# Optimization experiments

Measured on AMD Instinct MI355X. Metric: run time of the kernel, lower is better.

## Reference

```python
import jax, jax.numpy as jnp
import numpy as np

N = 50000   # num nodes
E = 600000  # num edges per signed adjacency
D = 128     # feature dim
K = 10      # num_diff_layers
C = 0.15    # restart probability


def setup_inputs() -> dict:
    key = jax.random.key(0)
    ks = jax.random.split(key, 8)
    rows_p = jax.random.randint(ks[0], (E,), 0, N, dtype=jnp.int32)
    cols_p = jax.random.randint(ks[1], (E,), 0, N, dtype=jnp.int32)
    vals_p = jax.random.uniform(ks[2], (E,), dtype=jnp.float32)
    rows_m = jax.random.randint(ks[3], (E,), 0, N, dtype=jnp.int32)
    cols_m = jax.random.randint(ks[4], (E,), 0, N, dtype=jnp.int32)
    vals_m = jax.random.uniform(ks[5], (E,), dtype=jnp.float32)
    X = jax.random.normal(ks[6], (N, D), dtype=jnp.float32)
    # torch code draws old_M ~ Uniform(-1, 1) at forward time; we expose it as input
    M0 = jax.random.uniform(ks[7], (N, D), dtype=jnp.float32, minval=-1.0, maxval=1.0)
    return {"rows_p": rows_p, "cols_p": cols_p, "vals_p": vals_p,
            "rows_m": rows_m, "cols_m": cols_m, "vals_m": vals_m,
            "X": X, "M0": M0}


def _spmm(rows, cols, vals, dense):
    # COO sparse [N,N] @ dense [N,D]: gather columns, scale, scatter-add to rows
    return jax.ops.segment_sum(vals[:, None] * dense[cols], rows,
                               num_segments=dense.shape[0])


def reference(rows_p, cols_p, vals_p, rows_m, cols_m, vals_m, X, M0):
    tilda_X = C * X  # restart term
    P, M = X, M0
    for _ in range(K):
        new_P = _spmm(rows_p, cols_p, vals_p, P) + _spmm(rows_m, cols_m, vals_m, M) + tilda_X
        new_M = _spmm(rows_m, cols_m, vals_m, P) + _spmm(rows_p, cols_p, vals_p, M)
        P, M = new_P, new_M
    return (P, M)
```

## Files before the change

kernel.cpp:

```cpp
#include <hip/hip_runtime.h>
#include <math.h>


#define TB 256

__device__ __forceinline__ unsigned pack_bf16(float a, float b) {
    unsigned ua = __float_as_uint(a), ub = __float_as_uint(b);
    ua += 0x7fffu + ((ua >> 16) & 1u);
    ub += 0x7fffu + ((ub >> 16) & 1u);
    return (ua >> 16) | (ub & 0xffff0000u);
}

__device__ __forceinline__ float2 unpack_bf16(unsigned w) {
    float2 r;
    r.x = __uint_as_float(w << 16);
    r.y = __uint_as_float(w & 0xffff0000u);
    return r;
}

__global__ void zero_int_kernel(int* __restrict__ p, int n) {
    int i = blockIdx.x * blockDim.x + threadIdx.x;
    if (i < n) p[i] = 0;
}

__global__ void hist2_kernel(const int* __restrict__ rows_p, const int* __restrict__ rows_m,
                             int E, int* __restrict__ cnt) {
    int e = blockIdx.x * blockDim.x + threadIdx.x;
    if (e < 2 * E) {
        int r = (e < E) ? rows_p[e] : rows_m[e - E];
        atomicAdd(&cnt[r], 1);
    }
}

__global__ void scanA_kernel(const int* __restrict__ cnt, int* __restrict__ bsum, int n) {
    __shared__ int wsum[16];
    int tid = threadIdx.x, lane = tid & 63, wid = tid >> 6;
    int i = blockIdx.x * 1024 + tid;
    int x = (i < n) ? cnt[i] : 0;
#pragma unroll
    for (int o = 1; o < 64; o <<= 1) { int y = __shfl_up(x, o); if (lane >= o) x += y; }
    if (lane == 63) wsum[wid] = x;
    __syncthreads();
    if (tid == 0) {
        int s = 0;
#pragma unroll
        for (int w = 0; w < 16; ++w) s += wsum[w];
        bsum[blockIdx.x] = s;
    }
}

__global__ void scanB_kernel(int* __restrict__ bsum, int nb) {
    __shared__ int wsum[16];
    int tid = threadIdx.x, lane = tid & 63, wid = tid >> 6;
    int x = (tid < nb) ? bsum[tid] : 0;
    int incl = x;
#pragma unroll
    for (int o = 1; o < 64; o <<= 1) { int y = __shfl_up(incl, o); if (lane >= o) incl += y; }
    if (lane == 63) wsum[wid] = incl;
    __syncthreads();
    if (wid == 0) {
        int s = (lane < 16) ? wsum[lane] : 0;
#pragma unroll
        for (int o = 1; o < 16; o <<= 1) { int y = __shfl_up(s, o); if (lane >= o) s += y; }
        if (lane < 16) wsum[lane] = s;
    }
    __syncthreads();
    int base = (wid > 0) ? wsum[wid - 1] : 0;
    if (tid < nb) bsum[tid] = base + incl - x;
}

__global__ void scanC_kernel(const int* __restrict__ cnt, const int* __restrict__ bsum,
                             int* __restrict__ off, int* __restrict__ cur, int n) {
    __shared__ int wsum[16];
    int tid = threadIdx.x, lane = tid & 63, wid = tid >> 6;
    int i = blockIdx.x * 1024 + tid;
    int x = (i < n) ? cnt[i] : 0;
    int incl = x;
#pragma unroll
    for (int o = 1; o < 64; o <<= 1) { int y = __shfl_up(incl, o); if (lane >= o) incl += y; }
    if (lane == 63) wsum[wid] = incl;
    __syncthreads();
    if (wid == 0) {
        int s = (lane < 16) ? wsum[lane] : 0;
#pragma unroll
        for (int o = 1; o < 16; o <<= 1) { int y = __shfl_up(s, o); if (lane >= o) s += y; }
        if (lane < 16) wsum[lane] = s;
    }
    __syncthreads();
    int base = bsum[blockIdx.x] + ((wid > 0) ? wsum[wid - 1] : 0);
    if (i < n) {
        int ex = base + incl - x;
        off[i] = ex;
        cur[i] = ex;
        if (i == n - 1) off[n] = base + incl;
    }
}

__global__ void fill2_kernel(const int* __restrict__ rows_p, const int* __restrict__ cols_p,
                             const float* __restrict__ vals_p,
                             const int* __restrict__ rows_m, const int* __restrict__ cols_m,
                             const float* __restrict__ vals_m, int E,
                             int* __restrict__ cur, int2* __restrict__ edge) {
    int e = blockIdx.x * blockDim.x + threadIdx.x;
    if (e < 2 * E) {
        int r, c; float v;
        if (e < E) { r = rows_p[e]; c = cols_p[e]; v =  vals_p[e]; }
        else       { r = rows_m[e - E]; c = cols_m[e - E]; v = -vals_m[e - E]; }
        int p = atomicAdd(&cur[r], 1);
        edge[p] = make_int2(c, __float_as_int(v));
    }
}

__global__ void init_kernel(const float* __restrict__ X, const float* __restrict__ M0,
                            unsigned* __restrict__ Sb, unsigned* __restrict__ Db,
                            unsigned* __restrict__ tXb, int n) {
    int i = blockIdx.x * blockDim.x + threadIdx.x;
    if (i < n) {
        float2 x = ((const float2*)X)[i];
        float2 m = ((const float2*)M0)[i];
        Sb[i]  = pack_bf16(x.x + m.x, x.y + m.y);
        Db[i]  = pack_bf16(x.x - m.x, x.y - m.y);
        tXb[i] = pack_bf16(0.15f * x.x, 0.15f * x.y);
    }
}

__global__ void final_kernel(const unsigned* __restrict__ Sb, const unsigned* __restrict__ Db,
                             float* __restrict__ P, float* __restrict__ M, int n) {
    int i = blockIdx.x * blockDim.x + threadIdx.x;
    if (i < n) {
        float2 s = unpack_bf16(Sb[i]);
        float2 d = unpack_bf16(Db[i]);
        ((float2*)P)[i] = make_float2(0.5f * (s.x + d.x), 0.5f * (s.y + d.y));
        ((float2*)M)[i] = make_float2(0.5f * (s.x - d.x), 0.5f * (s.y - d.y));
    }
}

__global__ __launch_bounds__(TB) void layer_kernel(
    const int* __restrict__ off, const int2* __restrict__ edge,
    const unsigned* __restrict__ Sin, const unsigned* __restrict__ Din,
    unsigned* __restrict__ Sout, unsigned* __restrict__ Dout,
    const unsigned* __restrict__ tXb, int N) {
    int b = blockIdx.x;
    int slot = b & 7;
    int sys = slot >> 2;
    int r4 = (b >> 3) * 4 + (slot & 3);
    int row = r4 * 4 + (threadIdx.x >> 6);
    if (row >= N) return;
    int lane = threadIdx.x & 63;
    const unsigned* __restrict__ In  = sys ? Din : Sin;
    unsigned* __restrict__       Out = sys ? Dout : Sout;

    int ridx = row * 64 + lane;
    float2 t = unpack_bf16(tXb[ridx]);
    float ax = t.x, ay = t.y;

    int bg = off[row], e = off[row + 1];
    int j = bg;
    for (; j + 8 <= e; j += 8) {
        int2 e0 = edge[j],     e1 = edge[j + 1], e2 = edge[j + 2], e3 = edge[j + 3];
        int2 e4 = edge[j + 4], e5 = edge[j + 5], e6 = edge[j + 6], e7 = edge[j + 7];
        unsigned w0 = In[e0.x * 64 + lane];
        unsigned w1 = In[e1.x * 64 + lane];
        unsigned w2 = In[e2.x * 64 + lane];
        unsigned w3 = In[e3.x * 64 + lane];
        unsigned w4 = In[e4.x * 64 + lane];
        unsigned w5 = In[e5.x * 64 + lane];
        unsigned w6 = In[e6.x * 64 + lane];
        unsigned w7 = In[e7.x * 64 + lane];
        float v0 = __int_as_float(e0.y), v1 = __int_as_float(e1.y);
        float v2 = __int_as_float(e2.y), v3 = __int_as_float(e3.y);
        float v4 = __int_as_float(e4.y), v5 = __int_as_float(e5.y);
        float v6 = __int_as_float(e6.y), v7 = __int_as_float(e7.y);
        if (!sys) {
            v0 = fabsf(v0); v1 = fabsf(v1); v2 = fabsf(v2); v3 = fabsf(v3);
            v4 = fabsf(v4); v5 = fabsf(v5); v6 = fabsf(v6); v7 = fabsf(v7);
        }
        float2 g0 = unpack_bf16(w0), g1 = unpack_bf16(w1);
        float2 g2 = unpack_bf16(w2), g3 = unpack_bf16(w3);
        float2 g4 = unpack_bf16(w4), g5 = unpack_bf16(w5);
        float2 g6 = unpack_bf16(w6), g7 = unpack_bf16(w7);
        ax += v0 * g0.x + v1 * g1.x + v2 * g2.x + v3 * g3.x
            + v4 * g4.x + v5 * g5.x + v6 * g6.x + v7 * g7.x;
        ay += v0 * g0.y + v1 * g1.y + v2 * g2.y + v3 * g3.y
            + v4 * g4.y + v5 * g5.y + v6 * g6.y + v7 * g7.y;
    }
    for (; j < e; ++j) {
        int2 ed = edge[j];
        float v = __int_as_float(ed.y);
        if (!sys) v = fabsf(v);
        float2 g = unpack_bf16(In[ed.x * 64 + lane]);
        ax += v * g.x;
        ay += v * g.y;
    }
    Out[ridx] = pack_bf16(ax, ay);
}

extern "C" void kernel_launch(void* const* d_in, const int* in_sizes, int n_in,
                              void* d_out, int out_size, void* d_ws, size_t ws_size,
                              hipStream_t stream) {
    const int*   rows_p = (const int*)d_in[0];
    const int*   cols_p = (const int*)d_in[1];
    const float* vals_p = (const float*)d_in[2];
    const int*   rows_m = (const int*)d_in[3];
    const int*   cols_m = (const int*)d_in[4];
    const float* vals_m = (const float*)d_in[5];
    const float* X      = (const float*)d_in[6];
    const float* M0     = (const float*)d_in[7];

    const int E = in_sizes[0];
    const int D = 128;
    const int N = in_sizes[6] / D;
    const int K = 10;
    const int E2 = 2 * E;
    const size_t ND = (size_t)N * D;
    const int NP = (int)(ND / 2);

    float* outP = (float*)d_out;
    float* outM = outP + ND;

    char* ws = (char*)d_ws;
    size_t o = 0;
    auto alloc = [&](size_t b) -> void* {
        void* p = ws + o;
        o += (b + 255) & ~(size_t)255;
        return p;
    };
    unsigned* SbA  = (unsigned*)alloc((size_t)NP * 4);
    unsigned* DbA  = (unsigned*)alloc((size_t)NP * 4);
    unsigned* SbB  = (unsigned*)alloc((size_t)NP * 4);
    unsigned* DbB  = (unsigned*)alloc((size_t)NP * 4);
    unsigned* tXb  = (unsigned*)alloc((size_t)NP * 4);
    int*      cnt  = (int*)alloc((size_t)N * sizeof(int));
    int*      off  = (int*)alloc((size_t)(N + 1) * sizeof(int));
    int*      cur  = (int*)alloc((size_t)N * sizeof(int));
    int*      bsum = (int*)alloc(1024 * sizeof(int));
    int2*     edge = (int2*)alloc((size_t)E2 * sizeof(int2));

    int gN  = (N + TB - 1) / TB;
    int gE2 = (E2 + TB - 1) / TB;
    int gNP = (NP + TB - 1) / TB;
    int nb  = (N + 1023) / 1024;

    zero_int_kernel<<<gN, TB, 0, stream>>>(cnt, N);
    hist2_kernel<<<gE2, TB, 0, stream>>>(rows_p, rows_m, E, cnt);
    scanA_kernel<<<nb, 1024, 0, stream>>>(cnt, bsum, N);
    scanB_kernel<<<1, 1024, 0, stream>>>(bsum, nb);
    scanC_kernel<<<nb, 1024, 0, stream>>>(cnt, bsum, off, cur, N);
    fill2_kernel<<<gE2, TB, 0, stream>>>(rows_p, cols_p, vals_p,
                                         rows_m, cols_m, vals_m, E, cur, edge);

    init_kernel<<<gNP, TB, 0, stream>>>(X, M0, SbA, DbA, tXb, NP);

    int blocks_per_sys = (N + 3) / 4;
    int gridx = ((blocks_per_sys + 3) / 4) * 8;
    unsigned *Si = SbA, *Di = DbA, *So = SbB, *Do = DbB;
    for (int k = 0; k < K; ++k) {
        layer_kernel<<<gridx, TB, 0, stream>>>(off, edge, Si, Di, So, Do, tXb, N);
        unsigned* t;
        t = Si; Si = So; So = t;
        t = Di; Di = Do; Do = t;
    }

    final_kernel<<<gNP, TB, 0, stream>>>(Si, Di, outP, outM, NP);
}
```

Measured before the change: 1.158 ms.

## Interleave S and D features per row so one wavefront processes both systems

The separate S and D bf16 buffers are merged into one row-interleaved buffer: each row holds the 32 S words followed by the 32 D words. One 64-lane wavefront now handles a row for both systems. Lanes 0-31 take abs values (S) and lanes 32-63 take signed values (D), with each lane loading 8 bytes. This halves the edge-list and offset reads and makes each neighbour gather one contiguous 512-byte access instead of two separate ones. The inner unroll drops from 8 to 4 edges, which cuts memory-level parallelism per wave, and init/final are rewritten to use float4 accesses on the new layout.

```diff
diff --git a/kernel.cpp b/kernel.cpp
--- a/kernel.cpp
+++ b/kernel.cpp
@@ -112,87 +112,82 @@
 }
 
 __global__ void init_kernel(const float* __restrict__ X, const float* __restrict__ M0,
-                            unsigned* __restrict__ Sb, unsigned* __restrict__ Db,
-                            unsigned* __restrict__ tXb, int n) {
+                            uint2* __restrict__ SD, uint2* __restrict__ tXb, int n32) {
     int i = blockIdx.x * blockDim.x + threadIdx.x;
-    if (i < n) {
-        float2 x = ((const float2*)X)[i];
-        float2 m = ((const float2*)M0)[i];
-        Sb[i]  = pack_bf16(x.x + m.x, x.y + m.y);
-        Db[i]  = pack_bf16(x.x - m.x, x.y - m.y);
-        tXb[i] = pack_bf16(0.15f * x.x, 0.15f * x.y);
-    }
-}
-
-__global__ void final_kernel(const unsigned* __restrict__ Sb, const unsigned* __restrict__ Db,
-                             float* __restrict__ P, float* __restrict__ M, int n) {
+    if (i < n32) {
+        int r = i >> 5, q = i & 31;
+        float4 x = ((const float4*)X)[(size_t)r * 32 + q];
+        float4 m = ((const float4*)M0)[(size_t)r * 32 + q];
+        SD[(size_t)r * 64 + q]      = make_uint2(pack_bf16(x.x + m.x, x.y + m.y),
+                                                 pack_bf16(x.z + m.z, x.w + m.w));
+        SD[(size_t)r * 64 + 32 + q] = make_uint2(pack_bf16(x.x - m.x, x.y - m.y),
+                                                 pack_bf16(x.z - m.z, x.w - m.w));
+        tXb[(size_t)r * 32 + q]     = make_uint2(pack_bf16(0.15f * x.x, 0.15f * x.y),
+                                                 pack_bf16(0.15f * x.z, 0.15f * x.w));
+    }
+}
+
+__global__ void final_kernel(const uint2* __restrict__ SD,
+                             float* __restrict__ P, float* __restrict__ M, int n32) {
     int i = blockIdx.x * blockDim.x + threadIdx.x;
-    if (i < n) {
-        float2 s = unpack_bf16(Sb[i]);
-        float2 d = unpack_bf16(Db[i]);
-        ((float2*)P)[i] = make_float2(0.5f * (s.x + d.x), 0.5f * (s.y + d.y));
-        ((float2*)M)[i] = make_float2(0.5f * (s.x - d.x), 0.5f * (s.y - d.y));
+    if (i < n32) {
+        int r = i >> 5, q = i & 31;
+        uint2 ws = SD[(size_t)r * 64 + q];
+        uint2 wd = SD[(size_t)r * 64 + 32 + q];
+        float2 s0 = unpack_bf16(ws.x), s1 = unpack_bf16(ws.y);
+        float2 d0 = unpack_bf16(wd.x), d1 = unpack_bf16(wd.y);
+        float4 p4 = make_float4(0.5f * (s0.x + d0.x), 0.5f * (s0.y + d0.y),
+                                0.5f * (s1.x + d1.x), 0.5f * (s1.y + d1.y));
+        float4 m4 = make_float4(0.5f * (s0.x - d0.x), 0.5f * (s0.y - d0.y),
+                                0.5f * (s1.x - d1.x), 0.5f * (s1.y - d1.y));
+        ((float4*)P)[(size_t)r * 32 + q] = p4;
+        ((float4*)M)[(size_t)r * 32 + q] = m4;
     }
 }
 
 __global__ __launch_bounds__(TB) void layer_kernel(
     const int* __restrict__ off, const int2* __restrict__ edge,
-    const unsigned* __restrict__ Sin, const unsigned* __restrict__ Din,
-    unsigned* __restrict__ Sout, unsigned* __restrict__ Dout,
-    const unsigned* __restrict__ tXb, int N) {
-    int b = blockIdx.x;
-    int slot = b & 7;
-    int sys = slot >> 2;
-    int r4 = (b >> 3) * 4 + (slot & 3);
-    int row = r4 * 4 + (threadIdx.x >> 6);
+    const uint2* __restrict__ In, uint2* __restrict__ Out,
+    const uint2* __restrict__ tXb, int N) {
+    int row = blockIdx.x * 4 + (threadIdx.x >> 6);
     if (row >= N) return;
     int lane = threadIdx.x & 63;
-    const unsigned* __restrict__ In  = sys ? Din : Sin;
-    unsigned* __restrict__       Out = sys ? Dout : Sout;
-
-    int ridx = row * 64 + lane;
-    float2 t = unpack_bf16(tXb[ridx]);
-    float ax = t.x, ay = t.y;
+    int sel = lane >> 5;
+    int q = lane & 31;
+
+    uint2 t = tXb[(size_t)row * 32 + q];
+    float2 t0 = unpack_bf16(t.x), t1 = unpack_bf16(t.y);
+    float a0 = t0.x, a1 = t0.y, a2 = t1.x, a3 = t1.y;
 
     int bg = off[row], e = off[row + 1];
     int j = bg;
-    for (; j + 8 <= e; j += 8) {
-        int2 e0 = edge[j],     e1 = edge[j + 1], e2 = edge[j + 2], e3 = edge[j + 3];
-        int2 e4 = edge[j + 4], e5 = edge[j + 5], e6 = edge[j + 6], e7 = edge[j + 7];
-        unsigned w0 = In[e0.x * 64 + lane];
-        unsigned w1 = In[e1.x * 64 + lane];
-        unsigned w2 = In[e2.x * 64 + lane];
-        unsigned w3 = In[e3.x * 64 + lane];
-        unsigned w4 = In[e4.x * 64 + lane];
-        unsigned w5 = In[e5.x * 64 + lane];
-        unsigned w6 = In[e6.x * 64 + lane];
-        unsigned w7 = In[e7.x * 64 + lane];
+    for (; j + 4 <= e; j += 4) {
+        int2 e0 = edge[j], e1 = edge[j + 1], e2 = edge[j + 2], e3 = edge[j + 3];
+        uint2 w0 = In[(size_t)e0.x * 64 + lane];
+        uint2 w1 = In[(size_t)e1.x * 64 + lane];
+        uint2 w2 = In[(size_t)e2.x * 64 + lane];
+        uint2 w3 = In[(size_t)e3.x * 64 + lane];
         float v0 = __int_as_float(e0.y), v1 = __int_as_float(e1.y);
         float v2 = __int_as_float(e2.y), v3 = __int_as_float(e3.y);
-        float v4 = __int_as_float(e4.y), v5 = __int_as_float(e5.y);
-        float v6 = __int_as_float(e6.y), v7 = __int_as_float(e7.y);
-        if (!sys) {
-            v0 = fabsf(v0); v1 = fabsf(v1); v2 = fabsf(v2); v3 = fabsf(v3);
-            v4 = fabsf(v4); v5 = fabsf(v5); v6 = fabsf(v6); v7 = fabsf(v7);
-        }
-        float2 g0 = unpack_bf16(w0), g1 = unpack_bf16(w1);
-        float2 g2 = unpack_bf16(w2), g3 = unpack_bf16(w3);
-        float2 g4 = unpack_bf16(w4), g5 = unpack_bf16(w5);
-        float2 g6 = unpack_bf16(w6), g7 = unpack_bf16(w7);
-        ax += v0 * g0.x + v1 * g1.x + v2 * g2.x + v3 * g3.x
-            + v4 * g4.x + v5 * g5.x + v6 * g6.x + v7 * g7.x;
-        ay += v0 * g0.y + v1 * g1.y + v2 * g2.y + v3 * g3.y
-            + v4 * g4.y + v5 * g5.y + v6 * g6.y + v7 * g7.y;
+        if (!sel) { v0 = fabsf(v0); v1 = fabsf(v1); v2 = fabsf(v2); v3 = fabsf(v3); }
+        float2 g0a = unpack_bf16(w0.x), g0b = unpack_bf16(w0.y);
+        float2 g1a = unpack_bf16(w1.x), g1b = unpack_bf16(w1.y);
+        float2 g2a = unpack_bf16(w2.x), g2b = unpack_bf16(w2.y);
+        float2 g3a = unpack_bf16(w3.x), g3b = unpack_bf16(w3.y);
+        a0 += v0 * g0a.x + v1 * g1a.x + v2 * g2a.x + v3 * g3a.x;
+        a1 += v0 * g0a.y + v1 * g1a.y + v2 * g2a.y + v3 * g3a.y;
+        a2 += v0 * g0b.x + v1 * g1b.x + v2 * g2b.x + v3 * g3b.x;
+        a3 += v0 * g0b.y + v1 * g1b.y + v2 * g2b.y + v3 * g3b.y;
     }
     for (; j < e; ++j) {
         int2 ed = edge[j];
+        uint2 w = In[(size_t)ed.x * 64 + lane];
         float v = __int_as_float(ed.y);
-        if (!sys) v = fabsf(v);
-        float2 g = unpack_bf16(In[ed.x * 64 + lane]);
-        ax += v * g.x;
-        ay += v * g.y;
-    }
-    Out[ridx] = pack_bf16(ax, ay);
+        if (!sel) v = fabsf(v);
+        float2 ga = unpack_bf16(w.x), gb = unpack_bf16(w.y);
+        a0 += v * ga.x; a1 += v * ga.y; a2 += v * gb.x; a3 += v * gb.y;
+    }
+    Out[(size_t)row * 64 + lane] = make_uint2(pack_bf16(a0, a1), pack_bf16(a2, a3));
 }
 
 extern "C" void kernel_launch(void* const* d_in, const int* in_sizes, int n_in,
@@ -213,7 +208,7 @@
     const int K = 10;
     const int E2 = 2 * E;
     const size_t ND = (size_t)N * D;
-    const int NP = (int)(ND / 2);
+    const int N32 = N * 32;
 
     float* outP = (float*)d_out;
     float* outM = outP + ND;
@@ -225,21 +220,19 @@
         o += (b + 255) & ~(size_t)255;
         return p;
     };
-    unsigned* SbA  = (unsigned*)alloc((size_t)NP * 4);
-    unsigned* DbA  = (unsigned*)alloc((size_t)NP * 4);
-    unsigned* SbB  = (unsigned*)alloc((size_t)NP * 4);
-    unsigned* DbB  = (unsigned*)alloc((size_t)NP * 4);
-    unsigned* tXb  = (unsigned*)alloc((size_t)NP * 4);
-    int*      cnt  = (int*)alloc((size_t)N * sizeof(int));
-    int*      off  = (int*)alloc((size_t)(N + 1) * sizeof(int));
-    int*      cur  = (int*)alloc((size_t)N * sizeof(int));
-    int*      bsum = (int*)alloc(1024 * sizeof(int));
-    int2*     edge = (int2*)alloc((size_t)E2 * sizeof(int2));
-
-    int gN  = (N + TB - 1) / TB;
-    int gE2 = (E2 + TB - 1) / TB;
-    int gNP = (NP + TB - 1) / TB;
-    int nb  = (N + 1023) / 1024;
+    uint2* SDA  = (uint2*)alloc((size_t)N * 64 * 8);
+    uint2* SDB  = (uint2*)alloc((size_t)N * 64 * 8);
+    uint2* tXb  = (uint2*)alloc((size_t)N * 32 * 8);
+    int*   cnt  = (int*)alloc((size_t)N * sizeof(int));
+    int*   off  = (int*)alloc((size_t)(N + 1) * sizeof(int));
+    int*   cur  = (int*)alloc((size_t)N * sizeof(int));
+    int*   bsum = (int*)alloc(1024 * sizeof(int));
+    int2*  edge = (int2*)alloc((size_t)E2 * sizeof(int2));
+
+    int gN   = (N + TB - 1) / TB;
+    int gE2  = (E2 + TB - 1) / TB;
+    int gN32 = (N32 + TB - 1) / TB;
+    int nb   = (N + 1023) / 1024;
 
     zero_int_kernel<<<gN, TB, 0, stream>>>(cnt, N);
     hist2_kernel<<<gE2, TB, 0, stream>>>(rows_p, rows_m, E, cnt);
@@ -249,17 +242,14 @@
     fill2_kernel<<<gE2, TB, 0, stream>>>(rows_p, cols_p, vals_p,
                                          rows_m, cols_m, vals_m, E, cur, edge);
 
-    init_kernel<<<gNP, TB, 0, stream>>>(X, M0, SbA, DbA, tXb, NP);
-
-    int blocks_per_sys = (N + 3) / 4;
-    int gridx = ((blocks_per_sys + 3) / 4) * 8;
-    unsigned *Si = SbA, *Di = DbA, *So = SbB, *Do = DbB;
+    init_kernel<<<gN32, TB, 0, stream>>>(X, M0, SDA, tXb, N32);
+
+    int gL = (N + 3) / 4;
+    uint2 *Si = SDA, *So = SDB;
     for (int k = 0; k < K; ++k) {
-        layer_kernel<<<gridx, TB, 0, stream>>>(off, edge, Si, Di, So, Do, tXb, N);
-        unsigned* t;
-        t = Si; Si = So; So = t;
-        t = Di; Di = Do; Do = t;
-    }
-
-    final_kernel<<<gNP, TB, 0, stream>>>(Si, Di, outP, outM, NP);
-}
+        layer_kernel<<<gL, TB, 0, stream>>>(off, edge, Si, So, tXb, N);
+        uint2* t = Si; Si = So; So = t;
+    }
+
+    final_kernel<<<gN32, TB, 0, stream>>>(Si, outP, outM, N32);
+}
```

After: 1.087 ms. 6.1% less time.
